# Kernel tuning notes

Measured on AMD Instinct MI355X. Metric: run time of the kernel, lower is better.

## Reference

```python
import jax, jax.numpy as jnp
import numpy as np

SUB = 40   # subframe_size
NSUB = 4   # nb_subframes


def _glu(x, w):
    return x * jax.nn.sigmoid(x @ w.T)


def _gru(x, h, w_ih, w_hh):
    # torch.nn.GRUCell (bias=False): gates ordered r, z, n
    H = h.shape[-1]
    gi = x @ w_ih.T
    gh = h @ w_hh.T
    r = jax.nn.sigmoid(gi[:, :H] + gh[:, :H])
    z = jax.nn.sigmoid(gi[:, H:2 * H] + gh[:, H:2 * H])
    n = jnp.tanh(gi[:, 2 * H:] + r * gh[:, 2 * H:])
    return (1.0 - z) * n + z * h


def _fargan_forward(features, period, p):
    B, T, _ = features.shape
    period = jnp.clip(period, 32, 254)

    # ---- FARGANCond ----
    f = features[:, 2:, :]                               # [B, T-2, 20]
    pidx = jnp.clip(period[:, 2:] - 32, 0, 223)
    pe = p['pembed'][pidx]                               # [B, T-2, 12]
    x = jnp.tanh(jnp.concatenate([f, pe], -1) @ p['fd1_w'].T)   # [B, T-2, 64]
    y = jax.lax.conv_general_dilated(
        x.transpose(0, 2, 1), p['fconv1_w'], (1,), 'VALID',
        dimension_numbers=('NCH', 'OIH', 'NCH'))
    y = jnp.tanh(y).transpose(0, 2, 1)                   # [B, T-4, 128]
    cond = jnp.tanh(y @ p['fd2_w'].T)                    # [B, T-4, 320]

    nb_frames = T - 4
    cond_steps = cond.reshape(B, nb_frames, NSUB, 80)
    cond_steps = cond_steps.transpose(1, 2, 0, 3).reshape(nb_frames * NSUB, B, 80)
    pitch = period[:, 3:3 + nb_frames]                   # conv-center aligned pitch
    pitch_steps = jnp.repeat(pitch.T, NSUB, axis=0)      # [steps, B]

    rng = jnp.arange(SUB + 4)

    def step(carry, inp):
        exc_mem, prev_pred, s1, s2, s3, fwc_state = carry
        cond80, per = inp
        gain = 0.2 + 0.8 * jax.nn.sigmoid(cond80 @ p['cg_w'].T + p['cg_b'])
        gain = jnp.clip(gain, 0.001, 20.0)               # [B, 1]
        idx = 256 - per[:, None] + rng[None, :] - 2
        idx = idx - (idx >= 256) * per[:, None]
        idx = jnp.clip(idx, 0, 255)
        pred = jnp.take_along_axis(exc_mem, idx, axis=1) / (1e-5 + gain)  # [B, 44]
        prev = exc_mem[:, -SUB:] / (1e-5 + gain)         # [B, 40]
        tmp = jnp.concatenate([cond80, pred, prev], 1)   # [B, 164]
        fpitch = pred[:, 2:-2]                           # [B, 40]
        xcat = jnp.concatenate([fwc_state, tmp], 1)      # [B, 328]
        fwc_out = _glu(jnp.tanh(xcat @ p['fwc_w'].T), p['fwc_glu_w'])  # [B, 192]
        new_fwc_state = xcat[:, 164:]
        pg = jax.nn.sigmoid(fwc_out @ p['gout_w'].T + p['gout_b'])     # [B, 4]
        s1n = _gru(jnp.concatenate([fwc_out, pg[:, 0:1] * fpitch, prev], 1), s1, p['g1_ih'], p['g1_hh'])
        g1 = _glu(s1n, p['glu1_w'])
        s2n = _gru(jnp.concatenate([g1, pg[:, 1:2] * fpitch, prev], 1), s2, p['g2_ih'], p['g2_hh'])
        g2 = _glu(s2n, p['glu2_w'])
        s3n = _gru(jnp.concatenate([g2, pg[:, 2:3] * fpitch, prev], 1), s3, p['g3_ih'], p['g3_hh'])
        g3 = _glu(s3n, p['glu3_w'])
        skip_in = jnp.concatenate([g1, g2, g3, fwc_out, pg[:, 3:4] * fpitch, prev], 1)  # [B, 688+80]
        skip = _glu(jnp.tanh(skip_in @ p['skip_w'].T), p['skip_glu_w'])
        sig = jnp.tanh(skip @ p['sig_w'].T) * gain       # [B, 40]
        exc_mem = jnp.concatenate([exc_mem[:, SUB:], sig], 1)
        prev_pred = jnp.concatenate([prev_pred[:, SUB:], fpitch], 1)
        return (exc_mem, prev_pred, s1n, s2n, s3n, new_fwc_state), sig

    dt = features.dtype
    carry0 = (jnp.zeros((B, 256), dt), jnp.zeros((B, 256), dt),
              jnp.zeros((B, 160), dt), jnp.zeros((B, 128), dt),
              jnp.zeros((B, 128), dt), jnp.zeros((B, 164), dt))
    _, sigs = jax.lax.scan(jax.checkpoint(step), carry0, (cond_steps, pitch_steps))
    return sigs.transpose(1, 0, 2).reshape(B, -1)        # [B, nb_frames*160]


def _w(key, out_dim, in_dim):
    return jax.random.normal(key, (out_dim, in_dim), jnp.float32) / np.sqrt(in_dim)


def setup_inputs() -> dict:
    key = jax.random.key(0)
    ks = jax.random.split(key, 24)
    B, T = 128, 504
    d = {}
    d['features'] = jax.random.normal(ks[0], (B, T, 20), jnp.float32)
    d['period'] = jax.random.randint(ks[1], (B, T), 32, 255)
    d['pembed'] = jax.random.normal(ks[2], (224, 12), jnp.float32) * 0.3
    d['fd1_w'] = _w(ks[3], 64, 32)
    d['fconv1_w'] = jax.random.normal(ks[4], (128, 64, 3), jnp.float32) / np.sqrt(192.0)
    d['fd2_w'] = _w(ks[5], 320, 128)
    d['cg_w'] = _w(ks[6], 1, 80)
    d['cg_b'] = jnp.zeros((1,), jnp.float32)
    d['fwc_w'] = _w(ks[7], 192, 328)
    d['fwc_glu_w'] = _w(ks[8], 192, 192)
    d['g1_ih'] = _w(ks[9], 480, 272)
    d['g1_hh'] = _w(ks[10], 480, 160)
    d['glu1_w'] = _w(ks[11], 160, 160)
    d['g2_ih'] = _w(ks[12], 384, 240)
    d['g2_hh'] = _w(ks[13], 384, 128)
    d['glu2_w'] = _w(ks[14], 128, 128)
    d['g3_ih'] = _w(ks[15], 384, 208)
    d['g3_hh'] = _w(ks[16], 384, 128)
    d['glu3_w'] = _w(ks[17], 128, 128)
    d['skip_w'] = _w(ks[18], 128, 688)
    d['skip_glu_w'] = _w(ks[19], 128, 128)
    d['sig_w'] = _w(ks[20], 40, 128)
    d['gout_w'] = _w(ks[21], 4, 192)
    d['gout_b'] = jnp.zeros((4,), jnp.float32)
    return d


def reference(features, period, pembed, fd1_w, fconv1_w, fd2_w, cg_w, cg_b,
              fwc_w, fwc_glu_w, g1_ih, g1_hh, glu1_w, g2_ih, g2_hh, glu2_w,
              g3_ih, g3_hh, glu3_w, skip_w, skip_glu_w, sig_w, gout_w, gout_b):
    p = dict(pembed=pembed, fd1_w=fd1_w, fconv1_w=fconv1_w, fd2_w=fd2_w,
             cg_w=cg_w, cg_b=cg_b, fwc_w=fwc_w, fwc_glu_w=fwc_glu_w,
             g1_ih=g1_ih, g1_hh=g1_hh, glu1_w=glu1_w,
             g2_ih=g2_ih, g2_hh=g2_hh, glu2_w=glu2_w,
             g3_ih=g3_ih, g3_hh=g3_hh, glu3_w=glu3_w,
             skip_w=skip_w, skip_glu_w=skip_glu_w, sig_w=sig_w,
             gout_w=gout_w, gout_b=gout_b)
    return _fargan_forward(features, period, p)
```

## Files before the change

kernel.cpp:

```cpp
#include <hip/hip_runtime.h>
#include <hip/hip_fp16.h>
#include <math.h>


#define DEV __device__ __forceinline__

DEV float sigm(float x) { return 1.0f / (1.0f + __expf(-x)); }
DEV float tanh_f(float x) { return 1.0f - 2.0f / (__expf(2.0f * x) + 1.0f); }

typedef _Float16 h2v __attribute__((ext_vector_type(2)));

#if defined(__has_builtin)
#if __has_builtin(__builtin_amdgcn_fdot2)
#define HAVE_FDOT2 1
#endif
#endif

DEV float fdot2(h2v a, h2v b, float c) {
#ifdef HAVE_FDOT2
    return __builtin_amdgcn_fdot2(a, b, c, false);
#else
    return c + (float)a[0] * (float)b[0] + (float)a[1] * (float)b[1];
#endif
}

constexpr size_t STEPS = 2000;
constexpr size_t OFF_X     = 0;
constexpr size_t OFF_Y     = 4200000;
constexpr size_t OFF_GAIN  = 12392000;
constexpr size_t OFF_CONDH = 12648000;
constexpr size_t OFF_W     = 22888000;

constexpr size_t W_FWC     = 0;
constexpr size_t W_FWCGLU  = W_FWC    + 192*352;
constexpr size_t W_GOUT    = W_FWCGLU + 192*192;
constexpr size_t W_G1IH    = W_GOUT   + 4*192;
constexpr size_t W_G1HH    = W_G1IH   + 480*272;
constexpr size_t W_GLU1    = W_G1HH   + 480*160;
constexpr size_t W_G2IH    = W_GLU1   + 160*160;
constexpr size_t W_G2HH    = W_G2IH   + 384*240;
constexpr size_t W_GLU2    = W_G2HH   + 384*128;
constexpr size_t W_G3IH    = W_GLU2   + 128*128;
constexpr size_t W_G3HH    = W_G3IH   + 384*208;
constexpr size_t W_GLU3    = W_G3HH   + 384*128;
constexpr size_t W_SKIP    = W_GLU3   + 128*128;
constexpr size_t W_SKIPGLU = W_SKIP   + 128*704;
constexpr size_t W_SIG     = W_SKIPGLU+ 128*128;

__global__ void k_pack_h(const float* __restrict__ src, __half* __restrict__ dst,
                         int OUT, int K, int KP8) {
    int t = blockIdx.x * 256 + threadIdx.x;
    if (t >= OUT * KP8) return;
    int j = t % OUT;
    int k8 = t / OUT;
    __half* d = dst + (size_t)t * 8;
#pragma unroll
    for (int i = 0; i < 8; ++i) {
        int k = k8 * 8 + i;
        d[i] = (k < K) ? __float2half(src[(size_t)j * K + k]) : __float2half(0.0f);
    }
}

__global__ void k_feat(const float* __restrict__ features, const int* __restrict__ period,
                       const float* __restrict__ pembed, const float* __restrict__ fd1,
                       float* __restrict__ xbuf) {
    int t = blockIdx.x * 256 + threadIdx.x;
    const int total = 128 * 502 * 64;
    if (t >= total) return;
    int o = t & 63;
    int r = t >> 6;
    int ft = r % 502;
    int b = r / 502;
    const float* f = features + ((size_t)b * 504 + ft + 2) * 20;
    int per = period[b * 504 + ft + 2];
    per = min(max(per, 32), 254);
    const float* pe = pembed + (per - 32) * 12;
    const float* w = fd1 + o * 32;
    float acc = 0.0f;
#pragma unroll
    for (int i = 0; i < 20; ++i) acc += f[i] * w[i];
// ... 43 lines not shown
        for (int q = 0; q < 10; ++q) acc[q] += wv * yl[q * 128 + k];
    }
#pragma unroll
    for (int q = 0; q < 10; ++q)
        cond[((size_t)b * 500 + t0 + q) * 320 + tid] = __float2half(tanh_f(acc[q]));
}

__global__ void k_gain(const __half* __restrict__ cond, const float* __restrict__ cgw,
                       const float* __restrict__ cgb, float* __restrict__ gains) {
    int t = blockIdx.x * 256 + threadIdx.x;
    const int total = 128 * 2000;
    if (t >= total) return;
    int s = t % 2000;
    int b = t / 2000;
    int frame = s >> 2, sub = s & 3;
    const __half* c = cond + ((size_t)b * 500 + frame) * 320 + sub * 80;
    float acc = 0.0f;
#pragma unroll 8
    for (int i = 0; i < 80; ++i) acc += __half2float(c[i]) * cgw[i];
    float g = 0.2f + 0.8f * sigm(acc + cgb[0]);
    g = fminf(20.0f, fmaxf(0.001f, g));
    gains[t] = g;
}

DEV void dot8h(uint4 w, uint4 x, float& a0, float& a1) {
    const h2v* wv = (const h2v*)&w;
    const h2v* xv = (const h2v*)&x;
    a0 = fdot2(wv[0], xv[0], a0);
    a1 = fdot2(wv[1], xv[1], a1);
    a0 = fdot2(wv[2], xv[2], a0);
    a1 = fdot2(wv[3], xv[3], a1);
}

template <int OUT, int KP8, int S>
DEV void mv_partial(const uint4* __restrict__ WT, const __half* __restrict__ x,
                    float* __restrict__ part, int tid) {
    static_assert(KP8 % S == 0, "KP8 % S");
    static_assert(OUT * S <= 1024, "threads");
    constexpr int KS8 = KP8 / S;
    if (tid < OUT * S) {
        int j = tid % OUT;
        int sl = tid / OUT;
        const uint4* w = WT + (size_t)sl * KS8 * OUT + j;
        const uint4* xx = (const uint4*)x + (size_t)sl * KS8;
        float a0 = 0.0f, a1 = 0.0f;
#pragma unroll 4
        for (int k = 0; k < KS8; ++k) {
            dot8h(w[(size_t)k * OUT], xx[k], a0, a1);
        }
        part[tid] = a0 + a1;
    }
}

template <int OUT, int KP8A, int KP8B>
DEV void gru_partial(const uint4* __restrict__ wa, const __half* __restrict__ xa,
                     const uint4* __restrict__ wb, const __half* __restrict__ xb,
                     float* __restrict__ pa, float* __restrict__ pb, int tid) {
    static_assert((KP8A % 2 == 0) && (KP8B % 2 == 0), "even");
    constexpr int KA = KP8A / 2, KB = KP8B / 2;
    if (tid < OUT * 2) {
        int j = tid % OUT;
        int sl = tid / OUT;
        {
            const uint4* w = wa + (size_t)sl * KA * OUT + j;
            const uint4* xx = (const uint4*)xa + (size_t)sl * KA;
            float a0 = 0.0f, a1 = 0.0f;
#pragma unroll 4
            for (int k = 0; k < KA; ++k) dot8h(w[(size_t)k * OUT], xx[k], a0, a1);
            pa[tid] = a0 + a1;
        }
        {
            const uint4* w = wb + (size_t)sl * KB * OUT + j;
            const uint4* xx = (const uint4*)xb + (size_t)sl * KB;
            float b0 = 0.0f, b1 = 0.0f;
#pragma unroll 4
            for (int k = 0; k < KB; ++k) dot8h(w[(size_t)k * OUT], xx[k], b0, b1);
            pb[tid] = b0 + b1;
        }
    }
}

template <int H>
DEV void gru_update(const float* __restrict__ pa, const float* __restrict__ pb,
                    float* __restrict__ s, __half* __restrict__ sh, int tid) {
    constexpr int OUT = 3 * H;
    if (tid < H) {
        float gi_r = pa[tid] + pa[OUT + tid];
        float gh_r = pb[tid] + pb[OUT + tid];
        float gi_z = pa[H + tid] + pa[OUT + H + tid];
        float gh_z = pb[H + tid] + pb[OUT + H + tid];
        float gi_n = pa[2 * H + tid] + pa[OUT + 2 * H + tid];
        float gh_n = pb[2 * H + tid] + pb[OUT + 2 * H + tid];
        float r = sigm(gi_r + gh_r);
        float z = sigm(gi_z + gh_z);
        float n = tanh_f(gi_n + r * gh_n);
        float v = (1.0f - z) * n + z * s[tid];
        s[tid] = v;
        sh[tid] = __float2half(v);
    }
}

__global__ __launch_bounds__(1024) void fargan_main(const float* __restrict__ ws,
                                                    const int* __restrict__ period,
                                                    const float* __restrict__ goutb,
                                                    float* __restrict__ out) {
    const int b = blockIdx.x;
    const int tid = threadIdx.x;

    const __half* cond = (const __half*)(ws + OFF_CONDH);
    const float* gains = ws + OFF_GAIN;
    const __half* whb  = (const __half*)(ws + OFF_W);
    const uint4* wFWC     = (const uint4*)(whb + W_FWC);
    const uint4* wFWCGLU  = (const uint4*)(whb + W_FWCGLU);
    const uint4* wGOUT    = (const uint4*)(whb + W_GOUT);
    const uint4* wG1IH    = (const uint4*)(whb + W_G1IH);
    const uint4* wG1HH    = (const uint4*)(whb + W_G1HH);
    const uint4* wGLU1    = (const uint4*)(whb + W_GLU1);
    const uint4* wG2IH    = (const uint4*)(whb + W_G2IH);
    const uint4* wG2HH    = (const uint4*)(whb + W_G2HH);
    const uint4* wGLU2    = (const uint4*)(whb + W_GLU2);
    const uint4* wG3IH    = (const uint4*)(whb + W_G3IH);
    const uint4* wG3HH    = (const uint4*)(whb + W_G3HH);
    const uint4* wGLU3    = (const uint4*)(whb + W_GLU3);
    const uint4* wSKIP    = (const uint4*)(whb + W_SKIP);
    const uint4* wSKIPGLU = (const uint4*)(whb + W_SKIPGLU);
    const uint4* wSIG     = (const uint4*)(whb + W_SIG);

    __shared__ __align__(16) __half xcat_h[352];
    __shared__ __align__(16) __half inb_h[272];
    __shared__ __align__(16) __half fwcpre_h[192], fwcout_h[192];
    __shared__ __align__(16) __half s1_h[160], s2_h[128], s3_h[128];
    __shared__ __align__(16) __half g1_h[160], g2_h[128], g3_h[128];
    __shared__ __align__(16) __half skipin_h[704], skippre_h[128], skipout_h[128];
    __shared__ __align__(16) float exc[256];
    __shared__ __align__(16) float s1[160], s2[128], s3[128];
    __shared__ __align__(16) float partA[1024], partB[1024];
    __shared__ __align__(16) float fwcpre[192];
    __shared__ __align__(16) float pg[4];
    __shared__ __align__(16) float skippre[128];
    __shared__ __align__(16) float sigraw[40];

    for (int i = tid; i < 256; i += 1024) exc[i] = 0.0f;
    if (tid < 160) { s1[tid] = 0.0f; s1_h[tid] = __float2half(0.0f); }
    if (tid < 128) { s2[tid] = 0.0f; s3[tid] = 0.0f;
                     s2_h[tid] = __float2half(0.0f); s3_h[tid] = __float2half(0.0f); }
    if (tid < 164) xcat_h[tid] = __float2half(0.0f);
    if (tid >= 328 && tid < 352) xcat_h[tid] = __float2half(0.0f);
    if (tid >= 688 && tid < 704) skipin_h[tid] = __float2half(0.0f);
    __syncthreads();

    for (int s = 0; s < (int)STEPS; ++s) {
        const int frame = s >> 2;
        const float gain = gains[(size_t)b * 2000 + s];
        const float ig = 1.0f / (1e-5f + gain);
        int per = period[b * 504 + 3 + frame];
        per = min(max(per, 32), 254);

        if (tid < 80) {
            xcat_h[164 + tid] = cond[((size_t)b * 500 + frame) * 320 + (s & 3) * 80 + tid];
        } else if (tid >= 128 && tid < 172) {
            int j = tid - 128;
            int idx = 254 - per + j;
            if (idx >= 256) idx -= per;
            idx = min(255, max(0, idx));
            xcat_h[244 + j] = __float2half(exc[idx] * ig);
        } else if (tid >= 192 && tid < 232) {
            xcat_h[288 + tid - 192] = __float2half(exc[216 + tid - 192] * ig);
        }
        __syncthreads();

        mv_partial<192, 44, 4>(wFWC, xcat_h, partA, tid);
        __syncthreads();
        if (tid < 192) {
            float a = partA[tid] + partA[192 + tid] + partA[384 + tid] + partA[576 + tid];
            float t = tanh_f(a);
            fwcpre[tid] = t;
            fwcpre_h[tid] = __float2half(t);
        }
        __syncthreads();

        mv_partial<192, 24, 4>(wFWCGLU, fwcpre_h, partA, tid);
        if (tid >= 768 && tid < 800) {
            int t2 = tid - 768;
            int j = t2 & 3, sl = t2 >> 2;
            const uint4* w = wGOUT + (sl * 3) * 4 + j;
            const uint4* xx = (const uint4*)fwcpre_h + sl * 3;
            float a0 = 0.0f, a1 = 0.0f;
#pragma unroll
            for (int k = 0; k < 3; ++k) dot8h(w[k * 4], xx[k], a0, a1);
            partB[t2] = a0 + a1;
        } else if (tid >= 832 && tid < 996) {
            xcat_h[tid - 832] = xcat_h[tid - 832 + 164];
        }
        __syncthreads();

        if (tid < 192) {
            float a = partA[tid] + partA[192 + tid] + partA[384 + tid] + partA[576 + tid];
            float v = fwcpre[tid] * sigm(a);
            __half vh = __float2half(v);
            fwcout_h[tid] = vh;
            inb_h[tid] = vh;
        } else if (tid < 232) {
            float a = goutb[0];
#pragma unroll
            for (int sl = 0; sl < 8; ++sl) a += partB[sl * 4];
            inb_h[tid] = __float2half(sigm(a) * __half2float(xcat_h[246 + tid - 192]));
        } else if (tid < 272) {
            inb_h[tid] = xcat_h[288 + tid - 232];
        } else if (tid >= 960 && tid < 964) {
            int j = tid - 960;
            float a = goutb[j];
#pragma unroll
            for (int sl = 0; sl < 8; ++sl) a += partB[sl * 4 + j];
            pg[j] = sigm(a);
        }
        __syncthreads();

        gru_partial<480, 34, 20>(wG1IH, inb_h, wG1HH, s1_h, partA, partB, tid);
        __syncthreads();
        gru_update<160>(partA, partB, s1, s1_h, tid);
        __syncthreads();

        mv_partial<160, 20, 4>(wGLU1, s1_h, partA, tid);
        __syncthreads();
        if (tid < 160) {
            float a = partA[tid] + partA[160 + tid] + partA[320 + tid] + partA[480 + tid];
            float v = s1[tid] * sigm(a);
            __half vh = __float2half(v);
            g1_h[tid] = vh;
            inb_h[tid] = vh;
        } else if (tid < 200) {
            inb_h[tid] = __float2half(pg[1] * __half2float(xcat_h[246 + tid - 160]));
        } else if (tid < 240) {
            inb_h[tid] = xcat_h[288 + tid - 200];
        }
        __syncthreads();

        gru_partial<384, 30, 16>(wG2IH, inb_h, wG2HH, s2_h, partA, partB, tid);
        __syncthreads();
        gru_update<128>(partA, partB, s2, s2_h, tid);
        __syncthreads();

        mv_partial<128, 16, 8>(wGLU2, s2_h, partA, tid);
        __syncthreads();
        if (tid < 128) {
            float a = 0.0f;
#pragma unroll
            for (int sl = 0; sl < 8; ++sl) a += partA[sl * 128 + tid];
            float v = s2[tid] * sigm(a);
            __half vh = __float2half(v);
            g2_h[tid] = vh;
            inb_h[tid] = vh;
        } else if (tid < 168) {
            inb_h[tid] = __float2half(pg[2] * __half2float(xcat_h[246 + tid - 128]));
        } else if (tid < 208) {
            inb_h[tid] = xcat_h[288 + tid - 168];
        }
        __syncthreads();

        gru_partial<384, 26, 16>(wG3IH, inb_h, wG3HH, s3_h, partA, partB, tid);
        __syncthreads();
        gru_update<128>(partA, partB, s3, s3_h, tid);
        __syncthreads();

        mv_partial<128, 16, 8>(wGLU3, s3_h, partA, tid);
        __syncthreads();
        if (tid < 128) {
            float a = 0.0f;
#pragma unroll
            for (int sl = 0; sl < 8; ++sl) a += partA[sl * 128 + tid];
            float v = s3[tid] * sigm(a);
            __half vh = __float2half(v);
            g3_h[tid] = vh;
            skipin_h[288 + tid] = vh;
        } else if (tid < 288) {
            skipin_h[tid - 128] = g1_h[tid - 128];
        } else if (tid < 416) {
            skipin_h[160 + tid - 288] = g2_h[tid - 288];
        } else if (tid < 608) {
            skipin_h[tid] = fwcout_h[tid - 416];
        } else if (tid < 648) {
            skipin_h[tid] = __float2half(pg[3] * __half2float(xcat_h[246 + tid - 608]));
        } else if (tid < 688) {
            skipin_h[tid] = xcat_h[288 + tid - 648];
        }
        __syncthreads();

        mv_partial<128, 88, 8>(wSKIP, skipin_h, partA, tid);
        __syncthreads();
        if (tid < 128) {
            float a = 0.0f;
#pragma unroll
            for (int sl = 0; sl < 8; ++sl) a += partA[sl * 128 + tid];
            float t = tanh_f(a);
            skippre[tid] = t;
            skippre_h[tid] = __float2half(t);
        }
        __syncthreads();

        mv_partial<128, 16, 8>(wSKIPGLU, skippre_h, partA, tid);
        __syncthreads();
        if (tid < 128) {
            float a = 0.0f;
#pragma unroll
            for (int sl = 0; sl < 8; ++sl) a += partA[sl * 128 + tid];
            skipout_h[tid] = __float2half(skippre[tid] * sigm(a));
        }
        __syncthreads();

        mv_partial<40, 16, 8>(wSIG, skipout_h, partA, tid);
        __syncthreads();
        float keep = (tid < 216) ? exc[tid + 40] : 0.0f;
        if (tid < 40) {
            float a = 0.0f;
#pragma unroll
            for (int sl = 0; sl < 8; ++sl) a += partA[sl * 40 + tid];
            sigraw[tid] = tanh_f(a) * gain;
        }
        __syncthreads();
        if (tid < 216) {
            exc[tid] = keep;
        } else if (tid < 256) {
            float sv = sigraw[tid - 216];
            exc[tid] = sv;
            out[(size_t)b * 80000 + (size_t)s * 40 + (tid - 216)] = sv;
        }
        __syncthreads();
    }
}

extern "C" void kernel_launch(void* const* d_in, const int* in_sizes, int n_in,
                              void* d_out, int out_size, void* d_ws, size_t ws_size,
                              hipStream_t stream) {
    const float* features = (const float*)d_in[0];
    const int*   period   = (const int*)d_in[1];
    const float* pembed   = (const float*)d_in[2];
    const float* fd1_w    = (const float*)d_in[3];
    const float* fconv1_w = (const float*)d_in[4];
    const float* fd2_w    = (const float*)d_in[5];
    const float* cg_w     = (const float*)d_in[6];
    const float* cg_b     = (const float*)d_in[7];
    const float* fwc_w    = (const float*)d_in[8];
    const float* fwc_glu  = (const float*)d_in[9];
    const float* g1_ih    = (const float*)d_in[10];
    const float* g1_hh    = (const float*)d_in[11];
    const float* glu1_w   = (const float*)d_in[12];
    const float* g2_ih    = (const float*)d_in[13];
    const float* g2_hh    = (const float*)d_in[14];
    const float* glu2_w   = (const float*)d_in[15];
    const float* g3_ih    = (const float*)d_in[16];
    const float* g3_hh    = (const float*)d_in[17];
    const float* glu3_w   = (const float*)d_in[18];
    const float* skip_w   = (const float*)d_in[19];
    const float* skip_glu = (const float*)d_in[20];
    const float* sig_w    = (const float*)d_in[21];
    const float* gout_w   = (const float*)d_in[22];
    const float* gout_b   = (const float*)d_in[23];

// ... 41 lines not shown
```

Before: 36.20 ms.

## Prefetch next matvec weights into registers and cache G2 weights in LDS

Each matvec stage now issues global loads for the first few weight chunks of the following stage into registers before the barrier, so weight fetch latency overlaps with the current stage and the synchronisation. The G2 hidden-hidden and GLU2 weights are copied once into a 128KB shared-memory buffer and read from LDS on every step. This raises register pressure (up to 16 uint4 prefetch registers per thread) and LDS usage, which could reduce occupancy or cause spills, but the kernel likely runs a single block per CU anyway.

Measured after the change: 95.24 ms. 163% more time.

```diff
diff --git a/kernel.cpp b/kernel.cpp
--- a/kernel.cpp
+++ b/kernel.cpp
@@ -46,6 +46,10 @@
 constexpr size_t W_SKIP    = W_GLU3   + 128*128;
 constexpr size_t W_SKIPGLU = W_SKIP   + 128*704;
 constexpr size_t W_SIG     = W_SKIPGLU+ 128*128;
+
+constexpr int WL_G2HH = 0;
+constexpr int WL_GLU2 = 6144;
+constexpr int WL_TOT  = 8192;
 
 __global__ void k_pack_h(const float* __restrict__ src, __half* __restrict__ dst,
                          int OUT, int K, int KP8) {
@@ -155,48 +159,141 @@
     a1 = fdot2(wv[3], xv[3], a1);
 }
 
-template <int OUT, int KP8, int S>
-DEV void mv_partial(const uint4* __restrict__ WT, const __half* __restrict__ x,
-                    float* __restrict__ part, int tid) {
-    static_assert(KP8 % S == 0, "KP8 % S");
-    static_assert(OUT * S <= 1024, "threads");
+template <int OUT, int KP8, int S, int PF>
+DEV void mv_load(const uint4* __restrict__ WT, uint4* pf, int tid) {
     constexpr int KS8 = KP8 / S;
+    constexpr int P = (PF < KS8) ? PF : KS8;
+    if (tid < OUT * S) {
+        int j = tid % OUT;
+        int sl = tid / OUT;
+        const uint4* w = WT + (size_t)sl * KS8 * OUT + j;
+#pragma unroll
+        for (int k = 0; k < P; ++k) pf[k] = w[(size_t)k * OUT];
+    }
+}
+
+template <int OUT, int KP8, int S, int PF>
+DEV void mv_compute(const uint4* __restrict__ WT, const uint4* pf,
+                    const __half* __restrict__ x, float* __restrict__ part, int tid) {
+    constexpr int KS8 = KP8 / S;
+    constexpr int P = (PF < KS8) ? PF : KS8;
     if (tid < OUT * S) {
         int j = tid % OUT;
         int sl = tid / OUT;
         const uint4* w = WT + (size_t)sl * KS8 * OUT + j;
         const uint4* xx = (const uint4*)x + (size_t)sl * KS8;
         float a0 = 0.0f, a1 = 0.0f;
-#pragma unroll 4
-        for (int k = 0; k < KS8; ++k) {
-            dot8h(w[(size_t)k * OUT], xx[k], a0, a1);
-        }
+#pragma unroll
+        for (int k = 0; k < P; ++k) dot8h(pf[k], xx[k], a0, a1);
+#pragma unroll
+        for (int k = P; k < KS8; ++k) dot8h(w[(size_t)k * OUT], xx[k], a0, a1);
         part[tid] = a0 + a1;
     }
 }
 
-template <int OUT, int KP8A, int KP8B>
-DEV void gru_partial(const uint4* __restrict__ wa, const __half* __restrict__ xa,
-                     const uint4* __restrict__ wb, const __half* __restrict__ xb,
-                     float* __restrict__ pa, float* __restrict__ pb, int tid) {
-    static_assert((KP8A % 2 == 0) && (KP8B % 2 == 0), "even");
-    constexpr int KA = KP8A / 2, KB = KP8B / 2;
-    if (tid < OUT * 2) {
+template <int OUT, int KP8, int S>
+DEV void mv_compute_l(const uint4* wl, const __half* __restrict__ x,
+                      float* __restrict__ part, int tid) {
+    constexpr int KS8 = KP8 / S;
+    if (tid < OUT * S) {
         int j = tid % OUT;
         int sl = tid / OUT;
+        const uint4* w = wl + (size_t)sl * KS8 * OUT + j;
+        const uint4* xx = (const uint4*)x + (size_t)sl * KS8;
+        float a0 = 0.0f, a1 = 0.0f;
+#pragma unroll
+        for (int k = 0; k < KS8; ++k) dot8h(w[(size_t)k * OUT], xx[k], a0, a1);
+        part[tid] = a0 + a1;
+    }
+}
+
+template <int OUT, int KP8A, int KP8B, int PA, int PB>
+DEV void gru_load(const uint4* __restrict__ wa, const uint4* __restrict__ wb,
+                  uint4* pfa, uint4* pfb, int tid) {
+    constexpr int KA = KP8A / 2, KB = KP8B / 2;
+    constexpr int QA = (PA < KA) ? PA : KA;
+    constexpr int QB = (PB < KB) ? PB : KB;
+    if (tid < OUT * 2) {
+        int j = tid % OUT, sl = tid / OUT;
+        const uint4* w = wa + (size_t)sl * KA * OUT + j;
+#pragma unroll
+        for (int k = 0; k < QA; ++k) pfa[k] = w[(size_t)k * OUT];
+        const uint4* w2 = wb + (size_t)sl * KB * OUT + j;
+#pragma unroll
+        for (int k = 0; k < QB; ++k) pfb[k] = w2[(size_t)k * OUT];
+    }
+}
+
+template <int OUT, int KP8A, int PA>
+DEV void gru_load_a(const uint4* __restrict__ wa, uint4* pfa, int tid) {
+    constexpr int KA = KP8A / 2;
+    constexpr int QA = (PA < KA) ? PA : KA;
+    if (tid < OUT * 2) {
+        int j = tid % OUT, sl = tid / OUT;
+        const uint4* w = wa + (size_t)sl * KA * OUT + j;
+#pragma unroll
+        for (int k = 0; k < QA; ++k) pfa[k] = w[(size_t)k * OUT];
+    }
+}
+
+template <int OUT, int KP8A, int KP8B, int PA, int PB>
+DEV void gru_compute(const uint4* __restrict__ wa, const uint4* pfa,
+                     const __half* __restrict__ xa,
+                     const uint4* __restrict__ wb, const uint4* pfb,
+                     const __half* __restrict__ xb,
+                     float* __restrict__ pa, float* __restrict__ pb, int tid) {
+    constexpr int KA = KP8A / 2, KB = KP8B / 2;
+    constexpr int QA = (PA < KA) ? PA : KA;
+    constexpr int QB = (PB < KB) ? PB : KB;
+    if (tid < OUT * 2) {
+        int j = tid % OUT, sl = tid / OUT;
         {
             const uint4* w = wa + (size_t)sl * KA * OUT + j;
             const uint4* xx = (const uint4*)xa + (size_t)sl * KA;
             float a0 = 0.0f, a1 = 0.0f;
-#pragma unroll 4
-            for (int k = 0; k < KA; ++k) dot8h(w[(size_t)k * OUT], xx[k], a0, a1);
+#pragma unroll
+            for (int k = 0; k < QA; ++k) dot8h(pfa[k], xx[k], a0, a1);
+#pragma unroll
+            for (int k = QA; k < KA; ++k) dot8h(w[(size_t)k * OUT], xx[k], a0, a1);
             pa[tid] = a0 + a1;
         }
         {
             const uint4* w = wb + (size_t)sl * KB * OUT + j;
             const uint4* xx = (const uint4*)xb + (size_t)sl * KB;
             float b0 = 0.0f, b1 = 0.0f;
-#pragma unroll 4
+#pragma unroll
+            for (int k = 0; k < QB; ++k) dot8h(pfb[k], xx[k], b0, b1);
+#pragma unroll
+            for (int k = QB; k < KB; ++k) dot8h(w[(size_t)k * OUT], xx[k], b0, b1);
+            pb[tid] = b0 + b1;
+        }
+    }
+}
+
+template <int OUT, int KP8A, int KP8B, int PA>
+DEV void gru_compute_bl(const uint4* __restrict__ wa, const uint4* pfa,
+                        const __half* __restrict__ xa,
+                        const uint4* wl, const __half* __restrict__ xb,
+                        float* __restrict__ pa, float* __restrict__ pb, int tid) {
+    constexpr int KA = KP8A / 2, KB = KP8B / 2;
+    constexpr int QA = (PA < KA) ? PA : KA;
+    if (tid < OUT * 2) {
+        int j = tid % OUT, sl = tid / OUT;
+        {
+            const uint4* w = wa + (size_t)sl * KA * OUT + j;
+            const uint4* xx = (const uint4*)xa + (size_t)sl * KA;
+            float a0 = 0.0f, a1 = 0.0f;
+#pragma unroll
+            for (int k = 0; k < QA; ++k) dot8h(pfa[k], xx[k], a0, a1);
+#pragma unroll
+            for (int k = QA; k < KA; ++k) dot8h(w[(size_t)k * OUT], xx[k], a0, a1);
+            pa[tid] = a0 + a1;
+        }
+        {
+            const uint4* w = wl + (size_t)sl * KB * OUT + j;
+            const uint4* xx = (const uint4*)xb + (size_t)sl * KB;
+            float b0 = 0.0f, b1 = 0.0f;
+#pragma unroll
             for (int k = 0; k < KB; ++k) dot8h(w[(size_t)k * OUT], xx[k], b0, b1);
             pb[tid] = b0 + b1;
         }
@@ -249,6 +346,8 @@
     const uint4* wSKIPGLU = (const uint4*)(whb + W_SKIPGLU);
     const uint4* wSIG     = (const uint4*)(whb + W_SIG);
 
+    __shared__ __align__(16) uint4 wlds[WL_TOT];
+
     __shared__ __align__(16) __half xcat_h[352];
     __shared__ __align__(16) __half inb_h[272];
     __shared__ __align__(16) __half fwcpre_h[192], fwcout_h[192];
@@ -263,6 +362,9 @@
     __shared__ __align__(16) float skippre[128];
     __shared__ __align__(16) float sigraw[40];
 
+    for (int i = tid; i < 6144; i += 1024) wlds[WL_G2HH + i] = wG2HH[i];
+    for (int i = tid; i < 2048; i += 1024) wlds[WL_GLU2 + i] = wGLU2[i];
+
     for (int i = tid; i < 256; i += 1024) exc[i] = 0.0f;
     if (tid < 160) { s1[tid] = 0.0f; s1_h[tid] = __float2half(0.0f); }
     if (tid < 128) { s2[tid] = 0.0f; s3[tid] = 0.0f;
@@ -271,6 +373,9 @@
     if (tid >= 328 && tid < 352) xcat_h[tid] = __float2half(0.0f);
     if (tid >= 688 && tid < 704) skipin_h[tid] = __float2half(0.0f);
     __syncthreads();
+
+    uint4 pfA[8], pfB[4], pfF[4];
+    mv_load<192, 44, 4, 4>(wFWC, pfF, tid);
 
     for (int s = 0; s < (int)STEPS; ++s) {
         const int frame = s >> 2;
@@ -292,7 +397,8 @@
         }
         __syncthreads();
 
-        mv_partial<192, 44, 4>(wFWC, xcat_h, partA, tid);
+        mv_compute<192, 44, 4, 4>(wFWC, pfF, xcat_h, partA, tid);
+        mv_load<192, 24, 4, 8>(wFWCGLU, pfA, tid);
         __syncthreads();
         if (tid < 192) {
             float a = partA[tid] + partA[192 + tid] + partA[384 + tid] + partA[576 + tid];
@@ -302,7 +408,7 @@
         }
         __syncthreads();
 
-        mv_partial<192, 24, 4>(wFWCGLU, fwcpre_h, partA, tid);
+        mv_compute<192, 24, 4, 8>(wFWCGLU, pfA, fwcpre_h, partA, tid);
         if (tid >= 768 && tid < 800) {
             int t2 = tid - 768;
             int j = t2 & 3, sl = t2 >> 2;
@@ -315,6 +421,7 @@
         } else if (tid >= 832 && tid < 996) {
             xcat_h[tid - 832] = xcat_h[tid - 832 + 164];
         }
+        gru_load<480, 34, 20, 8, 4>(wG1IH, wG1HH, pfA, pfB, tid);
         __syncthreads();
 
         if (tid < 192) {
@@ -339,12 +446,15 @@
         }
         __syncthreads();
 
-        gru_partial<480, 34, 20>(wG1IH, inb_h, wG1HH, s1_h, partA, partB, tid);
+        gru_compute<480, 34, 20, 8, 4>(wG1IH, pfA, inb_h, wG1HH, pfB, s1_h,
+                                       partA, partB, tid);
+        mv_load<160, 20, 4, 8>(wGLU1, pfA, tid);
         __syncthreads();
         gru_update<160>(partA, partB, s1, s1_h, tid);
         __syncthreads();
 
-        mv_partial<160, 20, 4>(wGLU1, s1_h, partA, tid);
+        mv_compute<160, 20, 4, 8>(wGLU1, pfA, s1_h, partA, tid);
+        gru_load_a<384, 30, 8>(wG2IH, pfA, tid);
         __syncthreads();
         if (tid < 160) {
             float a = partA[tid] + partA[160 + tid] + partA[320 + tid] + partA[480 + tid];
@@ -359,12 +469,14 @@
         }
         __syncthreads();
 
-        gru_partial<384, 30, 16>(wG2IH, inb_h, wG2HH, s2_h, partA, partB, tid);
+        gru_compute_bl<384, 30, 16, 8>(wG2IH, pfA, inb_h, wlds + WL_G2HH, s2_h,
+                                       partA, partB, tid);
+        gru_load<384, 26, 16, 8, 4>(wG3IH, wG3HH, pfA, pfB, tid);
         __syncthreads();
         gru_update<128>(partA, partB, s2, s2_h, tid);
         __syncthreads();
 
-        mv_partial<128, 16, 8>(wGLU2, s2_h, partA, tid);
+        mv_compute_l<128, 16, 8>(wlds + WL_GLU2, s2_h, partA, tid);
         __syncthreads();
         if (tid < 128) {
             float a = 0.0f;
@@ -381,12 +493,15 @@
         }
         __syncthreads();
 
-        gru_partial<384, 26, 16>(wG3IH, inb_h, wG3HH, s3_h, partA, partB, tid);
+        gru_compute<384, 26, 16, 8, 4>(wG3IH, pfA, inb_h, wG3HH, pfB, s3_h,
+                                       partA, partB, tid);
+        mv_load<128, 16, 8, 2>(wGLU3, pfA, tid);
         __syncthreads();
         gru_update<128>(partA, partB, s3, s3_h, tid);
         __syncthreads();
 
-        mv_partial<128, 16, 8>(wGLU3, s3_h, partA, tid);
+        mv_compute<128, 16, 8, 2>(wGLU3, pfA, s3_h, partA, tid);
+        mv_load<128, 88, 8, 8>(wSKIP, pfA, tid);
         __syncthreads();
         if (tid < 128) {
             float a = 0.0f;
@@ -409,7 +524,8 @@
         }
         __syncthreads();
 
-        mv_partial<128, 88, 8>(wSKIP, skipin_h, partA, tid);
+        mv_compute<128, 88, 8, 8>(wSKIP, pfA, skipin_h, partA, tid);
+        mv_load<128, 16, 8, 2>(wSKIPGLU, pfA, tid);
         __syncthreads();
         if (tid < 128) {
             float a = 0.0f;
@@ -421,7 +537,8 @@
         }
         __syncthreads();
 
-        mv_partial<128, 16, 8>(wSKIPGLU, skippre_h, partA, tid);
+        mv_compute<128, 16, 8, 2>(wSKIPGLU, pfA, skippre_h, partA, tid);
+        mv_load<40, 16, 8, 2>(wSIG, pfA, tid);
         __syncthreads();
         if (tid < 128) {
             float a = 0.0f;
@@ -431,7 +548,8 @@
         }
         __syncthreads();
 
-        mv_partial<40, 16, 8>(wSIG, skipout_h, partA, tid);
+        mv_compute<40, 16, 8, 2>(wSIG, pfA, skipout_h, partA, tid);
+        mv_load<192, 44, 4, 4>(wFWC, pfF, tid);
         __syncthreads();
         float keep = (tid < 216) ? exc[tid + 40] : 0.0f;
         if (tid < 40) {
```

## Cache small GLU weights in LDS and G2 recurrent weights in registers

Applied to the files above, without the earlier changes.

Copies the FWC-GLU, GLU2 and GLU3 weight matrices (about 139 KB of fp16) into shared memory once before the step loop. It also preloads each thread's slice of the G2 hidden-to-hidden weights into eight uint4 registers. Per-step matrix-vector products then read these from LDS or registers instead of re-fetching from global memory or L2. This raises LDS use to near the per-block limit and adds register pressure, which could hurt occupancy or cause spills in a kernel already running 1024 threads per block.

After: 34.11 ms. 1.06x faster.

```diff
diff --git a/kernel.cpp b/kernel.cpp
--- a/kernel.cpp
+++ b/kernel.cpp
@@ -46,6 +46,11 @@
 constexpr size_t W_SKIP    = W_GLU3   + 128*128;
 constexpr size_t W_SKIPGLU = W_SKIP   + 128*704;
 constexpr size_t W_SIG     = W_SKIPGLU+ 128*128;
+
+constexpr int WL_FWCGLU = 0;
+constexpr int WL_GLU2   = 4608;
+constexpr int WL_GLU3   = 6656;
+constexpr int WL_TOT    = 8704;
 
 __global__ void k_pack_h(const float* __restrict__ src, __half* __restrict__ dst,
                          int OUT, int K, int KP8) {
@@ -168,9 +173,23 @@
         const uint4* xx = (const uint4*)x + (size_t)sl * KS8;
         float a0 = 0.0f, a1 = 0.0f;
 #pragma unroll 4
-        for (int k = 0; k < KS8; ++k) {
-            dot8h(w[(size_t)k * OUT], xx[k], a0, a1);
-        }
+        for (int k = 0; k < KS8; ++k) dot8h(w[(size_t)k * OUT], xx[k], a0, a1);
+        part[tid] = a0 + a1;
+    }
+}
+
+template <int OUT, int KP8, int S>
+DEV void mv_partial_l(const uint4* wl, const __half* __restrict__ x,
+                      float* __restrict__ part, int tid) {
+    constexpr int KS8 = KP8 / S;
+    if (tid < OUT * S) {
+        int j = tid % OUT;
+        int sl = tid / OUT;
+        const uint4* w = wl + (size_t)sl * KS8 * OUT + j;
+        const uint4* xx = (const uint4*)x + (size_t)sl * KS8;
+        float a0 = 0.0f, a1 = 0.0f;
+#pragma unroll
+        for (int k = 0; k < KS8; ++k) dot8h(w[(size_t)k * OUT], xx[k], a0, a1);
         part[tid] = a0 + a1;
     }
 }
@@ -249,6 +268,8 @@
     const uint4* wSKIPGLU = (const uint4*)(whb + W_SKIPGLU);
     const uint4* wSIG     = (const uint4*)(whb + W_SIG);
 
+    __shared__ __align__(16) uint4 wlds[WL_TOT];
+
     __shared__ __align__(16) __half xcat_h[352];
     __shared__ __align__(16) __half inb_h[272];
     __shared__ __align__(16) __half fwcpre_h[192], fwcout_h[192];
@@ -263,6 +284,22 @@
     __shared__ __align__(16) float skippre[128];
     __shared__ __align__(16) float sigraw[40];
 
+    for (int i = tid; i < 4608; i += 1024) wlds[WL_FWCGLU + i] = wFWCGLU[i];
+    for (int i = tid; i < 2048; i += 1024) wlds[WL_GLU2 + i] = wGLU2[i];
+    for (int i = tid; i < 2048; i += 1024) wlds[WL_GLU3 + i] = wGLU3[i];
+
+    const int j2 = tid % 384;
+    const int sl2 = (tid < 768) ? (tid / 384) : 0;
+    const uint4* g2b = wG2HH + (size_t)sl2 * 8 * 384 + j2;
+    const uint4 c0 = g2b[0 * 384];
+    const uint4 c1 = g2b[1 * 384];
+    const uint4 c2 = g2b[2 * 384];
+    const uint4 c3 = g2b[3 * 384];
+    const uint4 c4 = g2b[4 * 384];
+    const uint4 c5 = g2b[5 * 384];
+    const uint4 c6 = g2b[6 * 384];
+    const uint4 c7 = g2b[7 * 384];
+
     for (int i = tid; i < 256; i += 1024) exc[i] = 0.0f;
     if (tid < 160) { s1[tid] = 0.0f; s1_h[tid] = __float2half(0.0f); }
     if (tid < 128) { s2[tid] = 0.0f; s3[tid] = 0.0f;
@@ -302,7 +339,7 @@
         }
         __syncthreads();
 
-        mv_partial<192, 24, 4>(wFWCGLU, fwcpre_h, partA, tid);
+        mv_partial_l<192, 24, 4>(wlds + WL_FWCGLU, fwcpre_h, partA, tid);
         if (tid >= 768 && tid < 800) {
             int t2 = tid - 768;
             int j = t2 & 3, sl = t2 >> 2;
@@ -359,12 +396,35 @@
         }
         __syncthreads();
 
-        gru_partial<384, 30, 16>(wG2IH, inb_h, wG2HH, s2_h, partA, partB, tid);
+        if (tid < 768) {
+            constexpr int KA = 15;
+            {
+                const uint4* w = wG2IH + (size_t)sl2 * KA * 384 + j2;
+                const uint4* xx = (const uint4*)inb_h + (size_t)sl2 * KA;
+                float a0 = 0.0f, a1 = 0.0f;
+#pragma unroll 4
+                for (int k = 0; k < KA; ++k) dot8h(w[(size_t)k * 384], xx[k], a0, a1);
+                partA[tid] = a0 + a1;
+            }
+            {
+                const uint4* xb = (const uint4*)s2_h + (size_t)sl2 * 8;
+                float b0 = 0.0f, b1 = 0.0f;
+                dot8h(c0, xb[0], b0, b1);
+                dot8h(c1, xb[1], b0, b1);
+                dot8h(c2, xb[2], b0, b1);
+                dot8h(c3, xb[3], b0, b1);
+                dot8h(c4, xb[4], b0, b1);
+                dot8h(c5, xb[5], b0, b1);
+                dot8h(c6, xb[6], b0, b1);
+                dot8h(c7, xb[7], b0, b1);
+                partB[tid] = b0 + b1;
+            }
+        }
         __syncthreads();
         gru_update<128>(partA, partB, s2, s2_h, tid);
         __syncthreads();
 
-        mv_partial<128, 16, 8>(wGLU2, s2_h, partA, tid);
+        mv_partial_l<128, 16, 8>(wlds + WL_GLU2, s2_h, partA, tid);
         __syncthreads();
         if (tid < 128) {
             float a = 0.0f;
@@ -386,7 +446,7 @@
         gru_update<128>(partA, partB, s3, s3_h, tid);
         __syncthreads();
 
-        mv_partial<128, 16, 8>(wGLU3, s3_h, partA, tid);
+        mv_partial_l<128, 16, 8>(wlds + WL_GLU3, s3_h, partA, tid);
         __syncthreads();
         if (tid < 128) {
             float a = 0.0f;
```

## Restructure recurrent step with shuffle reductions, LDS-cached weights, and ring buffer

Applied to the files above, without the earlier changes.

Replaces the shared-memory partial-sum arrays and their separate reduction phases with warp-shuffle reductions inside each matrix-vector product. This removes several barriers per step. GRU input products are split into main/pitch/prev segments, so the gain scaling folds into the dot product and the inb_h staging is dropped. Small GLU weight matrices are cached in LDS with padded strides, and the excitation history becomes a ring buffer instead of being shifted each step. The cost is a large LDS footprint, which may limit occupancy and adds preload work, and the GRU stages no longer split K across threads.

New measurement: 116.0 ms. +220.3%, slower.

```diff
diff --git a/kernel.cpp b/kernel.cpp
--- a/kernel.cpp
+++ b/kernel.cpp
@@ -46,6 +46,11 @@
 constexpr size_t W_SKIP    = W_GLU3   + 128*128;
 constexpr size_t W_SKIPGLU = W_SKIP   + 128*704;
 constexpr size_t W_SIG     = W_SKIPGLU+ 128*128;
+
+constexpr int WL_FWCGLU = 0;
+constexpr int WL_GLU2   = 4612;
+constexpr int WL_GLU3   = 4612 + 2056;
+constexpr int WL_TOT    = 4612 + 2056 + 2056;
 
 __global__ void k_pack_h(const float* __restrict__ src, __half* __restrict__ dst,
                          int OUT, int K, int KP8) {
@@ -155,72 +160,64 @@
     a1 = fdot2(wv[3], xv[3], a1);
 }
 
-template <int OUT, int KP8, int S>
-DEV void mv_partial(const uint4* __restrict__ WT, const __half* __restrict__ x,
-                    float* __restrict__ part, int tid) {
-    static_assert(KP8 % S == 0, "KP8 % S");
-    static_assert(OUT * S <= 1024, "threads");
-    constexpr int KS8 = KP8 / S;
-    if (tid < OUT * S) {
-        int j = tid % OUT;
-        int sl = tid / OUT;
-        const uint4* w = WT + (size_t)sl * KS8 * OUT + j;
-        const uint4* xx = (const uint4*)x + (size_t)sl * KS8;
-        float a0 = 0.0f, a1 = 0.0f;
-#pragma unroll 4
-        for (int k = 0; k < KS8; ++k) {
-            dot8h(w[(size_t)k * OUT], xx[k], a0, a1);
-        }
-        part[tid] = a0 + a1;
-    }
-}
-
-template <int OUT, int KP8A, int KP8B>
-DEV void gru_partial(const uint4* __restrict__ wa, const __half* __restrict__ xa,
-                     const uint4* __restrict__ wb, const __half* __restrict__ xb,
-                     float* __restrict__ pa, float* __restrict__ pb, int tid) {
-    static_assert((KP8A % 2 == 0) && (KP8B % 2 == 0), "even");
-    constexpr int KA = KP8A / 2, KB = KP8B / 2;
-    if (tid < OUT * 2) {
-        int j = tid % OUT;
-        int sl = tid / OUT;
-        {
-            const uint4* w = wa + (size_t)sl * KA * OUT + j;
-            const uint4* xx = (const uint4*)xa + (size_t)sl * KA;
-            float a0 = 0.0f, a1 = 0.0f;
-#pragma unroll 4
-            for (int k = 0; k < KA; ++k) dot8h(w[(size_t)k * OUT], xx[k], a0, a1);
-            pa[tid] = a0 + a1;
-        }
-        {
-            const uint4* w = wb + (size_t)sl * KB * OUT + j;
-            const uint4* xx = (const uint4*)xb + (size_t)sl * KB;
-            float b0 = 0.0f, b1 = 0.0f;
-#pragma unroll 4
-            for (int k = 0; k < KB; ++k) dot8h(w[(size_t)k * OUT], xx[k], b0, b1);
-            pb[tid] = b0 + b1;
-        }
-    }
-}
-
-template <int H>
-DEV void gru_update(const float* __restrict__ pa, const float* __restrict__ pb,
-                    float* __restrict__ s, __half* __restrict__ sh, int tid) {
-    constexpr int OUT = 3 * H;
-    if (tid < H) {
-        float gi_r = pa[tid] + pa[OUT + tid];
-        float gh_r = pb[tid] + pb[OUT + tid];
-        float gi_z = pa[H + tid] + pa[OUT + H + tid];
-        float gh_z = pb[H + tid] + pb[OUT + H + tid];
-        float gi_n = pa[2 * H + tid] + pa[OUT + 2 * H + tid];
-        float gh_n = pb[2 * H + tid] + pb[OUT + 2 * H + tid];
-        float r = sigm(gi_r + gh_r);
-        float z = sigm(gi_z + gh_z);
-        float n = tanh_f(gi_n + r * gh_n);
-        float v = (1.0f - z) * n + z * s[tid];
-        s[tid] = v;
-        sh[tid] = __float2half(v);
-    }
+template <int OUT, int KP8, int LS>
+DEV float mv_red(const uint4* __restrict__ W, const __half* __restrict__ x, int tid) {
+    static_assert(KP8 % LS == 0, "KP8 % LS");
+    constexpr int KS8 = KP8 / LS;
+    const int j = tid / LS;
+    const int sl = tid % LS;
+    const uint4* w = W + (size_t)(sl * KS8) * OUT + j;
+    const uint4* xx = (const uint4*)x + sl * KS8;
+    float a0 = 0.0f, a1 = 0.0f;
+#pragma unroll
+    for (int k = 0; k < KS8; ++k) dot8h(w[(size_t)k * OUT], xx[k], a0, a1);
+    float a = a0 + a1;
+#pragma unroll
+    for (int m = LS / 2; m >= 1; m >>= 1) a += __shfl_xor(a, m, 64);
+    return a;
+}
+
+template <int OUT, int KP8, int LS>
+DEV float mv_red_l(const uint4* wl, const __half* __restrict__ x, int tid) {
+    constexpr int KS8 = KP8 / LS;
+    constexpr int STRIDE = KS8 * OUT + 1;
+    const int j = tid / LS;
+    const int sl = tid % LS;
+    const uint4* w = wl + sl * STRIDE + j;
+    const uint4* xx = (const uint4*)x + sl * KS8;
+    float a0 = 0.0f, a1 = 0.0f;
+#pragma unroll
+    for (int k = 0; k < KS8; ++k) dot8h(w[(size_t)k * OUT], xx[k], a0, a1);
+    float a = a0 + a1;
+#pragma unroll
+    for (int m = LS / 2; m >= 1; m >>= 1) a += __shfl_xor(a, m, 64);
+    return a;
+}
+
+template <int OUT, int C0>
+DEV float gru_gi(const uint4* __restrict__ W, const __half* __restrict__ xmain,
+                 const __half* __restrict__ pitch, const __half* __restrict__ prev,
+                 float pgv, int j) {
+    const uint4* xm = (const uint4*)xmain;
+    const uint4* xp = (const uint4*)pitch;
+    const uint4* xv = (const uint4*)prev;
+    float a0 = 0.0f, a1 = 0.0f, p0 = 0.0f, p1 = 0.0f;
+#pragma unroll
+    for (int k = 0; k < C0; ++k) dot8h(W[(size_t)k * OUT + j], xm[k], a0, a1);
+#pragma unroll
+    for (int k = 0; k < 5; ++k) dot8h(W[(size_t)(C0 + k) * OUT + j], xp[k], p0, p1);
+#pragma unroll
+    for (int k = 0; k < 5; ++k) dot8h(W[(size_t)(C0 + 5 + k) * OUT + j], xv[k], a0, a1);
+    return a0 + a1 + pgv * (p0 + p1);
+}
+
+template <int OUT, int CH>
+DEV float gru_gh(const uint4* __restrict__ W, const __half* __restrict__ s, int j) {
+    const uint4* xx = (const uint4*)s;
+    float b0 = 0.0f, b1 = 0.0f;
+#pragma unroll
+    for (int k = 0; k < CH; ++k) dot8h(W[(size_t)k * OUT + j], xx[k], b0, b1);
+    return b0 + b1;
 }
 
 __global__ __launch_bounds__(1024) void fargan_main(const float* __restrict__ ws,
@@ -249,31 +246,45 @@
     const uint4* wSKIPGLU = (const uint4*)(whb + W_SKIPGLU);
     const uint4* wSIG     = (const uint4*)(whb + W_SIG);
 
+    __shared__ __align__(16) uint4 wlds[WL_TOT];
+
     __shared__ __align__(16) __half xcat_h[352];
-    __shared__ __align__(16) __half inb_h[272];
     __shared__ __align__(16) __half fwcpre_h[192], fwcout_h[192];
     __shared__ __align__(16) __half s1_h[160], s2_h[128], s3_h[128];
-    __shared__ __align__(16) __half g1_h[160], g2_h[128], g3_h[128];
+    __shared__ __align__(16) __half g1_h[160], g2_h[128];
     __shared__ __align__(16) __half skipin_h[704], skippre_h[128], skipout_h[128];
-    __shared__ __align__(16) float exc[256];
+    __shared__ __align__(16) __half pitch_h[40];
+    __shared__ __align__(16) __half prev_h[56];
+    __shared__ __align__(16) float ring[256];
     __shared__ __align__(16) float s1[160], s2[128], s3[128];
-    __shared__ __align__(16) float partA[1024], partB[1024];
-    __shared__ __align__(16) float fwcpre[192];
-    __shared__ __align__(16) float pg[4];
-    __shared__ __align__(16) float skippre[128];
-    __shared__ __align__(16) float sigraw[40];
-
-    for (int i = tid; i < 256; i += 1024) exc[i] = 0.0f;
+    __shared__ __align__(16) float fwcpre[192], skippre[128];
+    __shared__ __align__(16) float gi_s[480], gh_s[480];
+    __shared__ __align__(16) float pg[4], goutb_l[4];
+
+    for (int i = tid; i < 4608; i += 1024) {
+        int sl = i / 1152, rem = i % 1152;
+        wlds[WL_FWCGLU + sl * 1153 + rem] = wFWCGLU[i];
+    }
+    for (int i = tid; i < 2048; i += 1024) {
+        int sl = i / 256, rem = i % 256;
+        wlds[WL_GLU2 + sl * 257 + rem] = wGLU2[i];
+        wlds[WL_GLU3 + sl * 257 + rem] = wGLU3[i];
+    }
+
+    for (int i = tid; i < 256; i += 1024) ring[i] = 0.0f;
     if (tid < 160) { s1[tid] = 0.0f; s1_h[tid] = __float2half(0.0f); }
     if (tid < 128) { s2[tid] = 0.0f; s3[tid] = 0.0f;
                      s2_h[tid] = __float2half(0.0f); s3_h[tid] = __float2half(0.0f); }
     if (tid < 164) xcat_h[tid] = __float2half(0.0f);
     if (tid >= 328 && tid < 352) xcat_h[tid] = __float2half(0.0f);
     if (tid >= 688 && tid < 704) skipin_h[tid] = __float2half(0.0f);
+    if (tid >= 704 && tid < 720) prev_h[tid - 704 + 40] = __float2half(0.0f);
+    if (tid < 4) goutb_l[tid] = goutb[tid];
     __syncthreads();
 
     for (int s = 0; s < (int)STEPS; ++s) {
         const int frame = s >> 2;
+        const int head = (s * 40) & 255;
         const float gain = gains[(size_t)b * 2000 + s];
         const float ig = 1.0f / (1e-5f + gain);
         int per = period[b * 504 + 3 + frame];
@@ -286,167 +297,175 @@
             int idx = 254 - per + j;
             if (idx >= 256) idx -= per;
             idx = min(255, max(0, idx));
-            xcat_h[244 + j] = __float2half(exc[idx] * ig);
+            xcat_h[244 + j] = __float2half(ring[(head + idx) & 255] * ig);
         } else if (tid >= 192 && tid < 232) {
-            xcat_h[288 + tid - 192] = __float2half(exc[216 + tid - 192] * ig);
-        }
-        __syncthreads();
-
-        mv_partial<192, 44, 4>(wFWC, xcat_h, partA, tid);
-        __syncthreads();
-        if (tid < 192) {
-            float a = partA[tid] + partA[192 + tid] + partA[384 + tid] + partA[576 + tid];
-            float t = tanh_f(a);
-            fwcpre[tid] = t;
-            fwcpre_h[tid] = __float2half(t);
-        }
-        __syncthreads();
-
-        mv_partial<192, 24, 4>(wFWCGLU, fwcpre_h, partA, tid);
-        if (tid >= 768 && tid < 800) {
+            int j = tid - 192;
+            xcat_h[288 + j] = __float2half(ring[(head + 216 + j) & 255] * ig);
+        }
+        __syncthreads();
+
+        if (tid < 768) {
+            float a = mv_red<192, 44, 4>(wFWC, xcat_h, tid);
+            if ((tid & 3) == 0) {
+                int j = tid >> 2;
+                float t = tanh_f(a);
+                fwcpre[j] = t;
+                fwcpre_h[j] = __float2half(t);
+            }
+        } else if (tid < 808) {
+            pitch_h[tid - 768] = xcat_h[246 + tid - 768];
+        } else if (tid < 848) {
+            prev_h[tid - 808] = xcat_h[288 + tid - 808];
+        }
+        __syncthreads();
+
+        if (tid < 768) {
+            float a = mv_red_l<192, 24, 4>(wlds + WL_FWCGLU, fwcpre_h, tid);
+            if ((tid & 3) == 0) {
+                int j = tid >> 2;
+                float v = fwcpre[j] * sigm(a);
+                __half vh = __float2half(v);
+                fwcout_h[j] = vh;
+                skipin_h[416 + j] = vh;
+            }
+        } else if (tid < 800) {
             int t2 = tid - 768;
-            int j = t2 & 3, sl = t2 >> 2;
-            const uint4* w = wGOUT + (sl * 3) * 4 + j;
-            const uint4* xx = (const uint4*)fwcpre_h + sl * 3;
+            int j = t2 >> 3, sl = t2 & 7;
+            const uint4* xx = (const uint4*)fwcpre_h;
             float a0 = 0.0f, a1 = 0.0f;
 #pragma unroll
-            for (int k = 0; k < 3; ++k) dot8h(w[k * 4], xx[k], a0, a1);
-            partB[t2] = a0 + a1;
+            for (int k = 0; k < 3; ++k) dot8h(wGOUT[(size_t)(sl * 3 + k) * 4 + j],
+                                              xx[sl * 3 + k], a0, a1);
+            float a = a0 + a1;
+            a += __shfl_xor(a, 1, 64);
+            a += __shfl_xor(a, 2, 64);
+            a += __shfl_xor(a, 4, 64);
+            if (sl == 0) pg[j] = sigm(a + goutb_l[j]);
         } else if (tid >= 832 && tid < 996) {
             xcat_h[tid - 832] = xcat_h[tid - 832 + 164];
         }
         __syncthreads();
 
-        if (tid < 192) {
-            float a = partA[tid] + partA[192 + tid] + partA[384 + tid] + partA[576 + tid];
-            float v = fwcpre[tid] * sigm(a);
-            __half vh = __float2half(v);
-            fwcout_h[tid] = vh;
-            inb_h[tid] = vh;
-        } else if (tid < 232) {
-            float a = goutb[0];
-#pragma unroll
-            for (int sl = 0; sl < 8; ++sl) a += partB[sl * 4];
-            inb_h[tid] = __float2half(sigm(a) * __half2float(xcat_h[246 + tid - 192]));
-        } else if (tid < 272) {
-            inb_h[tid] = xcat_h[288 + tid - 232];
-        } else if (tid >= 960 && tid < 964) {
-            int j = tid - 960;
-            float a = goutb[j];
-#pragma unroll
-            for (int sl = 0; sl < 8; ++sl) a += partB[sl * 4 + j];
-            pg[j] = sigm(a);
-        }
-        __syncthreads();
-
-        gru_partial<480, 34, 20>(wG1IH, inb_h, wG1HH, s1_h, partA, partB, tid);
-        __syncthreads();
-        gru_update<160>(partA, partB, s1, s1_h, tid);
-        __syncthreads();
-
-        mv_partial<160, 20, 4>(wGLU1, s1_h, partA, tid);
-        __syncthreads();
+        if (tid < 480) {
+            gi_s[tid] = gru_gi<480, 24>(wG1IH, fwcout_h, pitch_h, prev_h, pg[0], tid);
+        } else if (tid >= 512 && tid < 992) {
+            int j = tid - 512;
+            gh_s[j] = gru_gh<480, 20>(wG1HH, s1_h, j);
+        }
+        __syncthreads();
+
         if (tid < 160) {
-            float a = partA[tid] + partA[160 + tid] + partA[320 + tid] + partA[480 + tid];
-            float v = s1[tid] * sigm(a);
-            __half vh = __float2half(v);
-            g1_h[tid] = vh;
-            inb_h[tid] = vh;
-        } else if (tid < 200) {
-            inb_h[tid] = __float2half(pg[1] * __half2float(xcat_h[246 + tid - 160]));
-        } else if (tid < 240) {
-            inb_h[tid] = xcat_h[288 + tid - 200];
-        }
-        __syncthreads();
-
-        gru_partial<384, 30, 16>(wG2IH, inb_h, wG2HH, s2_h, partA, partB, tid);
-        __syncthreads();
-        gru_update<128>(partA, partB, s2, s2_h, tid);
-        __syncthreads();
-
-        mv_partial<128, 16, 8>(wGLU2, s2_h, partA, tid);
-        __syncthreads();
+            float r = sigm(gi_s[tid] + gh_s[tid]);
+            float z = sigm(gi_s[160 + tid] + gh_s[160 + tid]);
+            float n = tanh_f(gi_s[320 + tid] + r * gh_s[320 + tid]);
+            float v = (1.0f - z) * n + z * s1[tid];
+            s1[tid] = v;
+            s1_h[tid] = __float2half(v);
+        } else if (tid >= 256 && tid < 296) {
+            int jj = tid - 256;
+            skipin_h[608 + jj] = __float2half(pg[3] * __half2float(pitch_h[jj]));
+        } else if (tid >= 296 && tid < 336) {
+            skipin_h[648 + tid - 296] = prev_h[tid - 296];
+        }
+        __syncthreads();
+
+        if (tid < 640) {
+            float a = mv_red<160, 20, 4>(wGLU1, s1_h, tid);
+            if ((tid & 3) == 0) {
+                int j = tid >> 2;
+                float v = s1[j] * sigm(a);
+                __half vh = __float2half(v);
+                g1_h[j] = vh;
+                skipin_h[j] = vh;
+            }
+        }
+        __syncthreads();
+
+        if (tid < 384) {
+            gi_s[tid] = gru_gi<384, 20>(wG2IH, g1_h, pitch_h, prev_h, pg[1], tid);
+        } else if (tid < 768) {
+            int j = tid - 384;
+            gh_s[j] = gru_gh<384, 16>(wG2HH, s2_h, j);
+        }
+        __syncthreads();
+
         if (tid < 128) {
-            float a = 0.0f;
-#pragma unroll
-            for (int sl = 0; sl < 8; ++sl) a += partA[sl * 128 + tid];
-            float v = s2[tid] * sigm(a);
-            __half vh = __float2half(v);
-            g2_h[tid] = vh;
-            inb_h[tid] = vh;
-        } else if (tid < 168) {
-            inb_h[tid] = __float2half(pg[2] * __half2float(xcat_h[246 + tid - 128]));
-        } else if (tid < 208) {
-            inb_h[tid] = xcat_h[288 + tid - 168];
-        }
-        __syncthreads();
-
-        gru_partial<384, 26, 16>(wG3IH, inb_h, wG3HH, s3_h, partA, partB, tid);
-        __syncthreads();
-        gru_update<128>(partA, partB, s3, s3_h, tid);
-        __syncthreads();
-
-        mv_partial<128, 16, 8>(wGLU3, s3_h, partA, tid);
-        __syncthreads();
+            float r = sigm(gi_s[tid] + gh_s[tid]);
+            float z = sigm(gi_s[128 + tid] + gh_s[128 + tid]);
+            float n = tanh_f(gi_s[256 + tid] + r * gh_s[256 + tid]);
+            float v = (1.0f - z) * n + z * s2[tid];
+            s2[tid] = v;
+            s2_h[tid] = __float2half(v);
+        }
+        __syncthreads();
+
+        {
+            float a = mv_red_l<128, 16, 8>(wlds + WL_GLU2, s2_h, tid);
+            if ((tid & 7) == 0) {
+                int j = tid >> 3;
+                float v = s2[j] * sigm(a);
+                __half vh = __float2half(v);
+                g2_h[j] = vh;
+                skipin_h[160 + j] = vh;
+            }
+        }
+        __syncthreads();
+
+        if (tid < 384) {
+            gi_s[tid] = gru_gi<384, 16>(wG3IH, g2_h, pitch_h, prev_h, pg[2], tid);
+        } else if (tid < 768) {
+            int j = tid - 384;
+            gh_s[j] = gru_gh<384, 16>(wG3HH, s3_h, j);
+        }
+        __syncthreads();
+
         if (tid < 128) {
-            float a = 0.0f;
-#pragma unroll
-            for (int sl = 0; sl < 8; ++sl) a += partA[sl * 128 + tid];
-            float v = s3[tid] * sigm(a);
-            __half vh = __float2half(v);
-            g3_h[tid] = vh;
-            skipin_h[288 + tid] = vh;
-        } else if (tid < 288) {
-            skipin_h[tid - 128] = g1_h[tid - 128];
-        } else if (tid < 416) {
-            skipin_h[160 + tid - 288] = g2_h[tid - 288];
-        } else if (tid < 608) {
-            skipin_h[tid] = fwcout_h[tid - 416];
-        } else if (tid < 648) {
-            skipin_h[tid] = __float2half(pg[3] * __half2float(xcat_h[246 + tid - 608]));
-        } else if (tid < 688) {
-            skipin_h[tid] = xcat_h[288 + tid - 648];
-        }
-        __syncthreads();
-
-        mv_partial<128, 88, 8>(wSKIP, skipin_h, partA, tid);
-        __syncthreads();
-        if (tid < 128) {
-            float a = 0.0f;
-#pragma unroll
-            for (int sl = 0; sl < 8; ++sl) a += partA[sl * 128 + tid];
-            float t = tanh_f(a);
-            skippre[tid] = t;
-            skippre_h[tid] = __float2half(t);
-        }
-        __syncthreads();
-
-        mv_partial<128, 16, 8>(wSKIPGLU, skippre_h, partA, tid);
-        __syncthreads();
-        if (tid < 128) {
-            float a = 0.0f;
-#pragma unroll
-            for (int sl = 0; sl < 8; ++sl) a += partA[sl * 128 + tid];
-            skipout_h[tid] = __float2half(skippre[tid] * sigm(a));
-        }
-        __syncthreads();
-
-        mv_partial<40, 16, 8>(wSIG, skipout_h, partA, tid);
-        __syncthreads();
-        float keep = (tid < 216) ? exc[tid + 40] : 0.0f;
-        if (tid < 40) {
-            float a = 0.0f;
-#pragma unroll
-            for (int sl = 0; sl < 8; ++sl) a += partA[sl * 40 + tid];
-            sigraw[tid] = tanh_f(a) * gain;
-        }
-        __syncthreads();
-        if (tid < 216) {
-            exc[tid] = keep;
-        } else if (tid < 256) {
-            float sv = sigraw[tid - 216];
-            exc[tid] = sv;
-            out[(size_t)b * 80000 + (size_t)s * 40 + (tid - 216)] = sv;
+            float r = sigm(gi_s[tid] + gh_s[tid]);
+            float z = sigm(gi_s[128 + tid] + gh_s[128 + tid]);
+            float n = tanh_f(gi_s[256 + tid] + r * gh_s[256 + tid]);
+            float v = (1.0f - z) * n + z * s3[tid];
+            s3[tid] = v;
+            s3_h[tid] = __float2half(v);
+        }
+        __syncthreads();
+
+        {
+            float a = mv_red_l<128, 16, 8>(wlds + WL_GLU3, s3_h, tid);
+            if ((tid & 7) == 0) {
+                int j = tid >> 3;
+                skipin_h[288 + j] = __float2half(s3[j] * sigm(a));
+            }
+        }
+        __syncthreads();
+
+        {
+            float a = mv_red<128, 88, 8>(wSKIP, skipin_h, tid);
+            if ((tid & 7) == 0) {
+                int j = tid >> 3;
+                float t = tanh_f(a);
+                skippre[j] = t;
+                skippre_h[j] = __float2half(t);
+            }
+        }
+        __syncthreads();
+
+        {
+            float a = mv_red<128, 16, 8>(wSKIPGLU, skippre_h, tid);
+            if ((tid & 7) == 0) {
+                int j = tid >> 3;
+                skipout_h[j] = __float2half(skippre[j] * sigm(a));
+            }
+        }
+        __syncthreads();
+
+        if (tid < 320) {
+            float a = mv_red<40, 16, 8>(wSIG, skipout_h, tid);
+            if ((tid & 7) == 0) {
+                int j = tid >> 3;
+                float sv = tanh_f(a) * gain;
+                ring[(head + j) & 255] = sv;
+                out[(size_t)b * 80000 + (size_t)s * 40 + j] = sv;
+            }
         }
         __syncthreads();
     }
```
